# Kernel optimization log

Hardware: AMD Instinct MI355X
Metric: run time of the kernel (lower is better)

Reference implementation:

```python
import jax, jax.numpy as jnp
import numpy as np

B, T, I = 256, 384, 32      # batch, seq_len, input_size
M, D, O = 128, 64, 128      # ring positions, embedding_dim, num_outputs
K = 2                       # attention_radius -> 2K+1 = 5 neighbors
TEMP = 8.0                  # attention_temperature
EPS = 1e-5                  # torch LayerNorm default eps


def setup_inputs() -> dict:
    key = jax.random.key(0)
    ks = jax.random.split(key, 12)
    def lin(kw, kb, fan_in, shape_w, shape_b):
        lim = 1.0 / np.sqrt(fan_in)
        W = jax.random.uniform(kw, shape_w, jnp.float32, -lim, lim)
        b = jax.random.uniform(kb, shape_b, jnp.float32, -lim, lim)
        return W, b
    Wp, bp = lin(ks[0], ks[1], I, (I, D), (D,))
    Wg, bg = lin(ks[2], ks[3], D, (D, 1), (1,))
    Wo, bo = lin(ks[4], ks[5], D, (D, O), (O,))
    return {
        "x": jax.random.normal(ks[6], (B, T, I), jnp.float32),
        "ptr_init": jax.random.uniform(ks[7], (B,), jnp.float32) * M,
        "Wp": Wp, "bp": bp,
        "gamma": jnp.ones((D,), jnp.float32),
        "beta": jnp.zeros((D,), jnp.float32),
        "jump_dest": jax.random.uniform(ks[8], (M,), jnp.float32) * M,
        "Wg": Wg, "bg": bg,
        "ctx_strength": jnp.asarray(0.2, jnp.float32),
        "Wo": Wo, "bo": bo,
    }


def reference(x, ptr_init, Wp, bp, gamma, beta, jump_dest, Wg, bg, ctx_strength, Wo, bo):
    offsets = jnp.arange(-K, K + 1)               # [2K+1]
    bidx = jnp.arange(B)[:, None]                 # [B,1] batch index for gather/scatter
    half = M / 2.0
    ctx_scale = jax.nn.sigmoid(ctx_strength)

    def step(carry, x_t):
        ring, hidden, ptr = carry                 # [B,M,D], [B,D], [B]
        emb = jnp.tanh(x_t @ Wp + bp)             # input projection + activation
        # Gaussian attention over circular neighborhood of floor(ptr)
        base = jnp.clip(jnp.floor(ptr).astype(jnp.int32), 0, M - 1)
        idx = (base[:, None] + offsets[None, :]) % M            # [B,2K+1]
        delta = jnp.mod(idx.astype(ptr.dtype) - ptr[:, None] + half, M) - half
        w = jax.nn.softmax(-(delta ** 2) / TEMP, axis=1)        # [B,2K+1]
        neigh = ring[bidx, idx]                                  # gather [B,2K+1,D]
        ctx = jnp.sum(w[:, :, None] * neigh, axis=1)             # [B,D]
        state = jnp.tanh(emb + ctx_scale * ctx + hidden)
        # LayerNorm (biased variance, affine)
        mu = jnp.mean(state, axis=-1, keepdims=True)
        var = jnp.var(state, axis=-1, keepdims=True)
        hidden_new = (state - mu) * jax.lax.rsqrt(var + EPS) * gamma + beta
        # scatter-add weighted state back into the ring
        ring = ring.at[bidx, idx].add(w[:, :, None] * state[:, None, :])
        # pointer update: hard STE gate between learned jump and +1 walk
        cur = jnp.clip(ptr.astype(jnp.int32), 0, M - 1)
        jump_target = jump_dest[cur]
        jl = (state @ Wg + bg)[:, 0]
        probs = jax.nn.sigmoid(jl)
        gate = (probs > 0.5).astype(state.dtype) - jax.lax.stop_gradient(probs) + probs
        walk = (ptr + 1.0) % M
        ptr_new = jnp.where(gate > 0.5, jump_target, walk)
        return (ring, hidden_new, ptr_new), None

    ring0 = jnp.zeros((B, M, D), x.dtype)
    h0 = jnp.zeros((B, D), x.dtype)
    (ring, hidden, ptr), _ = jax.lax.scan(step, (ring0, h0, ptr_init), jnp.swapaxes(x, 0, 1))
    logits = hidden @ Wo + bo                     # [B, O]
    return logits
```

## Files before the change

kernel.cpp:

```cpp
#include <hip/hip_runtime.h>
#include <hip/hip_bf16.h>


#define BB 256
#define TT 384
#define II 32
#define MM 128
#define DD 64
#define OO 128
#define K2 0.1803368801f
#define PR 133
#define CHK 8
#define NCHK (TT / CHK)
#define NSLOT 6

__device__ __forceinline__ float bfbits(unsigned int lo16) {
    return __uint_as_float(lo16 << 16);
}
__device__ __forceinline__ float ldf(const void* p, long long i, bool isbf) {
    if (isbf) return bfbits((unsigned int)((const unsigned short*)p)[i]);
    return ((const float*)p)[i];
}

template <int CTRL>
__device__ __forceinline__ float dpp_add(float x) {
    int s = __builtin_amdgcn_update_dpp(0, __float_as_int(x), CTRL, 0xf, 0xf, true);
    return x + __int_as_float(s);
}
__device__ __forceinline__ void reduce3(float& a, float& b, float& c) {
    a = dpp_add<0x111>(a); b = dpp_add<0x111>(b); c = dpp_add<0x111>(c);
    a = dpp_add<0x112>(a); b = dpp_add<0x112>(b); c = dpp_add<0x112>(c);
    a = dpp_add<0x114>(a); b = dpp_add<0x114>(b); c = dpp_add<0x114>(c);
    a = dpp_add<0x118>(a); b = dpp_add<0x118>(b); c = dpp_add<0x118>(c);
    a = dpp_add<0x142>(a); b = dpp_add<0x142>(b); c = dpp_add<0x142>(c);
    a = dpp_add<0x143>(a); b = dpp_add<0x143>(b); c = dpp_add<0x143>(c);
    a = __int_as_float(__builtin_amdgcn_readlane(__float_as_int(a), 63));
    b = __int_as_float(__builtin_amdgcn_readlane(__float_as_int(b), 63));
    c = __int_as_float(__builtin_amdgcn_readlane(__float_as_int(c), 63));
}

__device__ __forceinline__ float fast_tanh(float x) {
    float e = __builtin_amdgcn_exp2f(x * 2.885390082f);
    return fmaf(-2.0f, __builtin_amdgcn_rcpf(e + 1.0f), 1.0f);
}

__global__ __launch_bounds__(256, 1)
void ring_fused(const void* __restrict__ x,
                const void* __restrict__ ptr_init,
                const void* __restrict__ Wp,
                const void* __restrict__ bp,
                const void* __restrict__ gamma,
                const void* __restrict__ beta,
                const void* __restrict__ jump_dest,
                const void* __restrict__ Wg,
                const void* __restrict__ bg,
                const void* __restrict__ cs,
                const void* __restrict__ Wo,
                const void* __restrict__ bo,
                void* __restrict__ out)
{
    __shared__ float ring[PR * DD];
    __shared__ float ebuf[NSLOT * CHK * DD];
    __shared__ float tab[MM * 8];
    __shared__ float hsh[DD];
    __shared__ int chunk_ready[NCHK];
    __shared__ int cons_done;

    const int tid = threadIdx.x;
    const int wid = tid >> 6;
    const int lane = tid & 63;
    const int b = blockIdx.x;
    const bool isbf = (((const unsigned int*)gamma)[0] == 0x3f803f80u);

    if (tid < NCHK) chunk_ready[tid] = 0;
    if (tid == 0) cons_done = 0;
    __syncthreads();

    if (wid != 0) {
        float wp[II];
        #pragma unroll
        for (int k = 0; k < II; k++) wp[k] = ldf(Wp, k * DD + lane, isbf);
        const float bpv = ldf(bp, lane, isbf);
        volatile int* vcd = &cons_done;

        for (int c = wid - 1; c < NCHK; c += 3) {
            while (*vcd < c - (NSLOT - 1)) __builtin_amdgcn_s_sleep(8);
            float* eslot = ebuf + (c % NSLOT) * (CHK * DD);
            #pragma unroll
            for (int k = 0; k < CHK; k++) {
                const size_t t = (size_t)c * CHK + k;
                float acc = bpv;
                if (isbf) {
                    const uint4* xr = (const uint4*)
                        ((const unsigned short*)x + ((size_t)b * TT + t) * II);
                    #pragma unroll
                    for (int q = 0; q < 4; q++) {
                        uint4 u = xr[q];
                        unsigned int uu[4] = {u.x, u.y, u.z, u.w};
                        #pragma unroll
                        for (int e = 0; e < 4; e++) {
                            acc = fmaf(bfbits(uu[e] & 0xffffu), wp[q * 8 + e * 2], acc);
                            acc = fmaf(bfbits(uu[e] >> 16),     wp[q * 8 + e * 2 + 1], acc);
                        }
                    }
                } else {
                    const float4* xr = (const float4*)
                        ((const float*)x + ((size_t)b * TT + t) * II);
                    #pragma unroll
                    for (int q = 0; q < II / 4; q++) {
                        float4 v = xr[q];
                        acc = fmaf(v.x, wp[q * 4 + 0], acc);
                        acc = fmaf(v.y, wp[q * 4 + 1], acc);
                        acc = fmaf(v.z, wp[q * 4 + 2], acc);
                        acc = fmaf(v.w, wp[q * 4 + 3], acc);
                    }
                }
                eslot[k * DD + lane] = fast_tanh(acc);
            }
            __threadfence_block();
            if (lane == 0) *(volatile int*)&chunk_ready[c] = 1;
        }
        return;
    }

    {
        float4 z4 = make_float4(0.f, 0.f, 0.f, 0.f);
        #pragma unroll
        for (int i = 0; i < 33; i++)
            ((float4*)ring)[lane + i * 64] = z4;
        ring[8448 + lane] = 0.0f;
    }

    const float gam = ldf(gamma, lane, isbf);
    const float bet = ldf(beta, lane, isbf);
    const float wgv = ldf(Wg, lane, isbf);
    const float bgv = ldf(bg, 0, isbf);
    const float csv = 1.0f / (1.0f + expf(-ldf(cs, 0, isbf)));

    #pragma unroll
    for (int h = 0; h < 2; h++) {
        const int m = lane + h * 64;
        const float jd = ldf(jump_dest, m, isbf);
        int bj = (int)jd; bj = min(bj, MM - 1);
        const float fj = jd - (float)bj;
        float e[5], se = 0.0f;
        #pragma unroll
        for (int j = 0; j < 5; j++) {
            const float dd = (float)(j - 2) - fj;
            e[j] = __builtin_amdgcn_exp2f(dd * dd * -K2);
            se += e[j];
        }
        const float inv = __builtin_amdgcn_rcpf(se);
        #pragma unroll
        for (int j = 0; j < 5; j++) tab[m * 8 + j] = e[j] * inv;
        tab[m * 8 + 5] = __int_as_float(bj);
    }

    const float p0 = ldf(ptr_init, b, isbf);
    int sbase = __builtin_amdgcn_readfirstlane(min(max((int)floorf(p0), 0), MM - 1));
    const float frac = p0 - (float)sbase;
    float w0, w1, w2, w3, w4;
    {
        float e[5], se = 0.0f;
        #pragma unroll
        for (int j = 0; j < 5; j++) {
            const float dd = (float)(j - 2) - frac;
            e[j] = __builtin_amdgcn_exp2f(dd * dd * -K2);
            se += e[j];
        }
        const float inv = __builtin_amdgcn_rcpf(se);
        w0 = e[0] * inv; w1 = e[1] * inv; w2 = e[2] * inv;
        w3 = e[3] * inv; w4 = e[4] * inv;
    }

    float nb0 = 0.f, nb1 = 0.f, nb2 = 0.f, nb3 = 0.f, nb4 = 0.f;
    float hid = 0.0f;
    volatile int* vcr = chunk_ready;

    for (int c = 0; c < NCHK; c++) {
        while (!vcr[c]) __builtin_amdgcn_s_sleep(1);
        const float* eslot = ebuf + (c % NSLOT) * (CHK * DD);

        float ev[CHK];
        #pragma unroll
        for (int j = 0; j < CHK; j++) ev[j] = eslot[j * DD + lane];

        #pragma unroll
        for (int k = 0; k < CHK; k++) {
            const float* ce = tab + (sbase << 3);
            const float c0 = ce[0], c1 = ce[1], c2 = ce[2],
                        c3 = ce[3], c4 = ce[4];
            const int bjc = __float_as_int(ce[5]);
            float* rb = ring + sbase * DD + lane;
            const float W5p = rb[5 * DD];

            const float ctx = fmaf(w0, nb0, fmaf(w1, nb1, 0.0f)) +
                              fmaf(w2, nb2, fmaf(w3, nb3, w4 * nb4));
            const float snn = fast_tanh(fmaf(csv, ctx, ev[k] + hid));

            float r0 = snn, r1 = snn * snn, r2 = snn * wgv;
            reduce3(r0, r1, r2);

            const float nv0 = fmaf(w0, snn, nb0), nv1 = fmaf(w1, snn, nb1),
                        nv2 = fmaf(w2, snn, nb2), nv3 = fmaf(w3, snn, nb3),
                        nv4 = fmaf(w4, snn, nb4);
            rb[0 * DD] = nv0; rb[1 * DD] = nv1; rb[2 * DD] = nv2;
            rb[3 * DD] = nv3; rb[4 * DD] = nv4;
            if (sbase <= 4 || sbase >= MM - 4) {
                const float nvv[5] = {nv0, nv1, nv2, nv3, nv4};
                #pragma unroll
                for (int j = 0; j < 5; j++) {
                    const int p = sbase + j;
                    if (p < 5)        ring[(p + MM) * DD + lane] = nvv[j];
                    else if (p >= MM) ring[(p - MM) * DD + lane] = nvv[j];
                }
            }

            const float mu = r0 * (1.0f / 64.0f);
            const float var = fmaf(-mu, mu, r1 * (1.0f / 64.0f));
            const float rstd = __builtin_amdgcn_rsqf(var + 1e-5f);
            hid = fmaf((snn - mu) * rstd, gam, bet);

            const float jl = r2 + bgv;
            const bool jump =
                __builtin_amdgcn_readfirstlane(__float_as_int(jl)) > 0;
            if (jump) {
                w0 = c0; w1 = c1; w2 = c2; w3 = c3; w4 = c4;
                sbase = __builtin_amdgcn_readfirstlane(bjc);
                const float* rj = ring + sbase * DD + lane;
                nb0 = rj[0 * DD]; nb1 = rj[1 * DD]; nb2 = rj[2 * DD];
                nb3 = rj[3 * DD]; nb4 = rj[4 * DD];
            } else {
                nb0 = nv1; nb1 = nv2; nb2 = nv3; nb3 = nv4; nb4 = W5p;
                sbase = (sbase + 1) & (MM - 1);
            }
        }
        if (lane == 0) *(volatile int*)&cons_done = c + 1;
    }

    hsh[lane] = hid;
    float a0 = ldf(bo, lane, isbf);
    float a1 = ldf(bo, lane + 64, isbf);
    #pragma unroll 8
    for (int d = 0; d < DD; d++) {
        const float h = hsh[d];
        a0 = fmaf(h, ldf(Wo, d * OO + lane, isbf), a0);
        a1 = fmaf(h, ldf(Wo, d * OO + lane + 64, isbf), a1);
    }
    if (isbf) {
        __hip_bfloat16* o = (__hip_bfloat16*)out;
        o[(size_t)b * OO + lane] = __float2bfloat16(a0);
        o[(size_t)b * OO + lane + 64] = __float2bfloat16(a1);
    } else {
        float* o = (float*)out;
        o[(size_t)b * OO + lane] = a0;
        o[(size_t)b * OO + lane + 64] = a1;
    }
}

extern "C" void kernel_launch(void* const* d_in, const int* in_sizes, int n_in,
                              void* d_out, int out_size, void* d_ws, size_t ws_size,
                              hipStream_t stream) {
    ring_fused<<<BB, 256, 0, stream>>>(
        d_in[0], d_in[1], d_in[2], d_in[3], d_in[4], d_in[5],
        d_in[6], d_in[7], d_in[8], d_in[9], d_in[10], d_in[11], d_out);
}
```

Baseline: 194.3 us.

## Speculatively precompute both jump and walk contexts to shorten the serial step chain

Restructures the per-timestep recurrence so the context sums for both the jump and walk successors are computed before the gate decision, then picked branch-free with selects. The self-contribution of the current state is folded in through a correction term. LayerNorm and tanh constants are also pre-scaled by log2(e)*2, and jump-destination indices are kept in registers and read with readlane instead of LDS. This is meant to take the LDS loads, the branch and the dot product off the serial dependency chain. The cost is extra redundant loads and arithmetic every step, and more register pressure.

Result: slower. 211.7 us (+8.9%).

```diff
diff --git a/kernel.cpp b/kernel.cpp
--- a/kernel.cpp
+++ b/kernel.cpp
@@ -9,6 +9,7 @@
 #define DD 64
 #define OO 128
 #define K2 0.1803368801f
+#define L2E2 2.885390082f
 #define PR 133
 #define CHK 8
 #define NCHK (TT / CHK)
@@ -40,7 +41,7 @@
 }
 
 __device__ __forceinline__ float fast_tanh(float x) {
-    float e = __builtin_amdgcn_exp2f(x * 2.885390082f);
+    float e = __builtin_amdgcn_exp2f(x * L2E2);
     return fmaf(-2.0f, __builtin_amdgcn_rcpf(e + 1.0f), 1.0f);
 }
 
@@ -59,9 +60,9 @@
                 const void* __restrict__ bo,
                 void* __restrict__ out)
 {
-    __shared__ float ring[PR * DD];
-    __shared__ float ebuf[NSLOT * CHK * DD];
-    __shared__ float tab[MM * 8];
+    __shared__ __align__(16) float ring[PR * DD];
+    __shared__ __align__(16) float ebuf[NSLOT * CHK * DD];
+    __shared__ __align__(16) float tab[MM * 8];
     __shared__ float hsh[DD];
     __shared__ int chunk_ready[NCHK];
     __shared__ int cons_done;
@@ -134,9 +135,13 @@
     const float gam = ldf(gamma, lane, isbf);
     const float bet = ldf(beta, lane, isbf);
     const float wgv = ldf(Wg, lane, isbf);
-    const float bgv = ldf(bg, 0, isbf);
+    const float bg64 = ldf(bg, 0, isbf) * (1.0f / 64.0f);
     const float csv = 1.0f / (1.0f + expf(-ldf(cs, 0, isbf)));
-
+    const float csv2 = csv * L2E2;
+    const float gam2 = gam * L2E2;
+    const float bet2 = bet * L2E2;
+
+    int tbj0 = 0, tbj1 = 0;
     #pragma unroll
     for (int h = 0; h < 2; h++) {
         const int m = lane + h * 64;
@@ -153,7 +158,7 @@
         const float inv = __builtin_amdgcn_rcpf(se);
         #pragma unroll
         for (int j = 0; j < 5; j++) tab[m * 8 + j] = e[j] * inv;
-        tab[m * 8 + 5] = __int_as_float(bj);
+        if (h == 0) tbj0 = bj; else tbj1 = bj;
     }
 
     const float p0 = ldf(ptr_init, b, isbf);
@@ -172,38 +177,57 @@
         w0 = e[0] * inv; w1 = e[1] * inv; w2 = e[2] * inv;
         w3 = e[3] * inv; w4 = e[4] * inv;
     }
+    int bjc;
+    {
+        const int bl = __builtin_amdgcn_readlane(tbj0, sbase & 63);
+        const int bh = __builtin_amdgcn_readlane(tbj1, sbase & 63);
+        bjc = (sbase & 64) ? bh : bl;
+    }
 
     float nb0 = 0.f, nb1 = 0.f, nb2 = 0.f, nb3 = 0.f, nb4 = 0.f;
-    float hid = 0.0f;
+    float snn = 0.f, dg = 0.f, rstd = 0.f;
+    float ctxpre = -bet2, scorr = 0.f;
+    float hid_raw = 0.f;
     volatile int* vcr = chunk_ready;
 
     for (int c = 0; c < NCHK; c++) {
         while (!vcr[c]) __builtin_amdgcn_s_sleep(1);
         const float* eslot = ebuf + (c % NSLOT) * (CHK * DD);
 
-        float ev[CHK];
-        #pragma unroll
-        for (int j = 0; j < CHK; j++) ev[j] = eslot[j * DD + lane];
+        float evb2[CHK];
+        #pragma unroll
+        for (int j = 0; j < CHK; j++)
+            evb2[j] = fmaf(eslot[j * DD + lane], L2E2, bet2);
 
         #pragma unroll
         for (int k = 0; k < CHK; k++) {
-            const float* ce = tab + (sbase << 3);
-            const float c0 = ce[0], c1 = ce[1], c2 = ce[2],
-                        c3 = ce[3], c4 = ce[4];
-            const int bjc = __float_as_int(ce[5]);
             float* rb = ring + sbase * DD + lane;
+            const float* jb = ring + bjc * DD + lane;
+            const float j0 = jb[0 * DD], j1 = jb[1 * DD], j2 = jb[2 * DD],
+                        j3 = jb[3 * DD], j4 = jb[4 * DD];
             const float W5p = rb[5 * DD];
-
-            const float ctx = fmaf(w0, nb0, fmaf(w1, nb1, 0.0f)) +
-                              fmaf(w2, nb2, fmaf(w3, nb3, w4 * nb4));
-            const float snn = fast_tanh(fmaf(csv, ctx, ev[k] + hid));
-
-            float r0 = snn, r1 = snn * snn, r2 = snn * wgv;
+            const float4 cvv = *(const float4*)(tab + (sbase << 3));
+            const float c4v = tab[(sbase << 3) + 4];
+
+            const int sb1 = (sbase + 1) & (MM - 1);
+            const int bwl = __builtin_amdgcn_readlane(tbj0, sb1 & 63);
+            const int bwh = __builtin_amdgcn_readlane(tbj1, sb1 & 63);
+            const int bjc_w = (sb1 & 64) ? bwh : bwl;
+            const int bjl = __builtin_amdgcn_readlane(tbj0, bjc & 63);
+            const int bjh = __builtin_amdgcn_readlane(tbj1, bjc & 63);
+            const int bjc_j = (bjc & 64) ? bjh : bjl;
+
+            const float A  = fmaf(dg, rstd, evb2[k]);
+            const float cx = fmaf(snn, scorr, ctxpre);
+            const float ex = __builtin_amdgcn_exp2f(A + cx);
+            const float sn = fmaf(-2.0f, __builtin_amdgcn_rcpf(ex + 1.0f), 1.0f);
+
+            float r0 = sn, r1 = sn * sn, r2 = fmaf(sn, wgv, bg64);
             reduce3(r0, r1, r2);
 
-            const float nv0 = fmaf(w0, snn, nb0), nv1 = fmaf(w1, snn, nb1),
-                        nv2 = fmaf(w2, snn, nb2), nv3 = fmaf(w3, snn, nb3),
-                        nv4 = fmaf(w4, snn, nb4);
+            const float nv0 = fmaf(w0, sn, nb0), nv1 = fmaf(w1, sn, nb1),
+                        nv2 = fmaf(w2, sn, nb2), nv3 = fmaf(w3, sn, nb3),
+                        nv4 = fmaf(w4, sn, nb4);
             rb[0 * DD] = nv0; rb[1 * DD] = nv1; rb[2 * DD] = nv2;
             rb[3 * DD] = nv3; rb[4 * DD] = nv4;
             if (sbase <= 4 || sbase >= MM - 4) {
@@ -216,36 +240,73 @@
                 }
             }
 
+            const float ctxwp = csv2 * fmaf(w0, nb1, fmaf(w1, nb2,
+                                 fmaf(w2, nb3, fmaf(w3, nb4, w4 * W5p))));
+            const float sww = csv2 * fmaf(w0, w1, fmaf(w1, w2,
+                                 fmaf(w2, w3, w3 * w4)));
+            const float ctxjp = csv2 * fmaf(cvv.x, j0, fmaf(cvv.y, j1,
+                                 fmaf(cvv.z, j2, fmaf(cvv.w, j3, c4v * j4))));
+
+            float ow0 = 0.f, ow1 = 0.f, ow2 = 0.f, ow3 = 0.f, ow4 = 0.f;
+            float sjc = 0.f;
+            {
+                int diff = bjc - sbase; if (diff < 0) diff += MM;
+                if (diff <= 4 || diff >= MM - 4) {
+                    #pragma unroll
+                    for (int i = 0; i < 5; i++) {
+                        int jj = diff + i; if (jj >= MM) jj -= MM;
+                        float wv = 0.0f;
+                        wv = (jj == 0) ? w0 : wv;
+                        wv = (jj == 1) ? w1 : wv;
+                        wv = (jj == 2) ? w2 : wv;
+                        wv = (jj == 3) ? w3 : wv;
+                        wv = (jj == 4) ? w4 : wv;
+                        if (i == 0) ow0 = wv; else if (i == 1) ow1 = wv;
+                        else if (i == 2) ow2 = wv; else if (i == 3) ow3 = wv;
+                        else ow4 = wv;
+                    }
+                    sjc = csv2 * fmaf(cvv.x, ow0, fmaf(cvv.y, ow1,
+                          fmaf(cvv.z, ow2, fmaf(cvv.w, ow3, c4v * ow4))));
+                }
+            }
+
             const float mu = r0 * (1.0f / 64.0f);
-            const float var = fmaf(-mu, mu, r1 * (1.0f / 64.0f));
-            const float rstd = __builtin_amdgcn_rsqf(var + 1e-5f);
-            hid = fmaf((snn - mu) * rstd, gam, bet);
-
-            const float jl = r2 + bgv;
-            const bool jump =
-                __builtin_amdgcn_readfirstlane(__float_as_int(jl)) > 0;
-            if (jump) {
-                w0 = c0; w1 = c1; w2 = c2; w3 = c3; w4 = c4;
-                sbase = __builtin_amdgcn_readfirstlane(bjc);
-                const float* rj = ring + sbase * DD + lane;
-                nb0 = rj[0 * DD]; nb1 = rj[1 * DD]; nb2 = rj[2 * DD];
-                nb3 = rj[3 * DD]; nb4 = rj[4 * DD];
-            } else {
-                nb0 = nv1; nb1 = nv2; nb2 = nv3; nb3 = nv4; nb4 = W5p;
-                sbase = (sbase + 1) & (MM - 1);
-            }
+            const float q  = fmaf(r1, 1.0f / 64.0f, 1e-5f);
+            const float va = fmaf(-mu, mu, q);
+            rstd = __builtin_amdgcn_rsqf(va);
+            const float d = sn - mu;
+            dg = d * gam2;
+            hid_raw = fmaf(d * rstd, gam, bet);
+
+            const bool jump = r2 > 0.0f;
+            ctxpre = jump ? ctxjp : ctxwp;
+            scorr  = jump ? sjc   : sww;
+            const float nj0 = fmaf(sn, ow0, j0), nj1 = fmaf(sn, ow1, j1),
+                        nj2 = fmaf(sn, ow2, j2), nj3 = fmaf(sn, ow3, j3),
+                        nj4 = fmaf(sn, ow4, j4);
+            nb0 = jump ? nj0 : nv1;
+            nb1 = jump ? nj1 : nv2;
+            nb2 = jump ? nj2 : nv3;
+            nb3 = jump ? nj3 : nv4;
+            nb4 = jump ? nj4 : W5p;
+            w0 = jump ? cvv.x : w0; w1 = jump ? cvv.y : w1;
+            w2 = jump ? cvv.z : w2; w3 = jump ? cvv.w : w3;
+            w4 = jump ? c4v   : w4;
+            sbase = jump ? bjc : sb1;
+            bjc   = jump ? bjc_j : bjc_w;
+            snn = sn;
         }
         if (lane == 0) *(volatile int*)&cons_done = c + 1;
     }
 
-    hsh[lane] = hid;
+    hsh[lane] = hid_raw;
     float a0 = ldf(bo, lane, isbf);
     float a1 = ldf(bo, lane + 64, isbf);
     #pragma unroll 8
-    for (int d = 0; d < DD; d++) {
-        const float h = hsh[d];
-        a0 = fmaf(h, ldf(Wo, d * OO + lane, isbf), a0);
-        a1 = fmaf(h, ldf(Wo, d * OO + lane + 64, isbf), a1);
+    for (int dd = 0; dd < DD; dd++) {
+        const float h = hsh[dd];
+        a0 = fmaf(h, ldf(Wo, dd * OO + lane, isbf), a0);
+        a1 = fmaf(h, ldf(Wo, dd * OO + lane + 64, isbf), a1);
     }
     if (isbf) {
         __hip_bfloat16* o = (__hip_bfloat16*)out;
```
